# Kernel optimization log

Measured on AMD Instinct MI355X. Metric: run time of the kernel, lower is better.

Reference implementation:

```python
import jax, jax.numpy as jnp
import numpy as np

B, T, X, H, Z = 64, 2048, 128, 256, 64


def setup_inputs() -> dict:
    key = jax.random.key(0)
    ks = jax.random.split(key, 6)
    s = lambda n: 1.0 / np.sqrt(n).astype(np.float32)
    return {
        "x_seq": jax.random.normal(ks[0], (B, T, X), jnp.float32),
        # LSTMCell params packed as [i|f|g|o] gates. Flax: input dense has no bias,
        # hidden dense has bias.
        "Wi": jax.random.normal(ks[1], (X, 4 * H), jnp.float32) * s(X),
        "Wh": jax.random.normal(ks[2], (H, 4 * H), jnp.float32) * s(H),
        "bh": jnp.zeros((4 * H,), jnp.float32),
        # head: Dense(H) -> relu -> Dense(2Z)
        "W1": jax.random.normal(ks[3], (H, H), jnp.float32) * s(H),
        "b1": jnp.zeros((H,), jnp.float32),
        "W2": jax.random.normal(ks[4], (H, 2 * Z), jnp.float32) * s(H),
        "b2": jnp.zeros((2 * Z,), jnp.float32),
    }


def _forward(x_seq, Wi, Wh, bh, W1, b1, W2, b2):
    Bsz = x_seq.shape[0]
    Hd = Wh.shape[0]
    # Precompute input projection for all timesteps (one big GEMM).
    x_proj = jnp.einsum('btx,xg->btg', x_seq, Wi)  # (B, T, 4H)
    xp = jnp.swapaxes(x_proj, 0, 1)  # (T, B, 4H) for scan

    def step(carry, xp_t):
        c, h = carry
        gates = xp_t + h @ Wh + bh  # (B, 4H)
        i, f, g, o = jnp.split(gates, 4, axis=-1)
        i = jax.nn.sigmoid(i)
        f = jax.nn.sigmoid(f)
        g = jnp.tanh(g)
        o = jax.nn.sigmoid(o)
        c = f * c + i * g
        h = o * jnp.tanh(c)
        hid = jax.nn.relu(h @ W1 + b1)
        out = hid @ W2 + b2  # (B, 2Z)
        return (c, h), out

    c0 = jnp.zeros((Bsz, Hd), x_seq.dtype)
    h0 = jnp.zeros((Bsz, Hd), x_seq.dtype)
    _, outs = jax.lax.scan(step, (c0, h0), xp)  # outs: (T, B, 2Z)
    outs = jnp.swapaxes(outs, 0, 1)  # (B, T, 2Z)
    mu_seq, log_sigma_seq = jnp.split(outs, 2, axis=-1)
    return mu_seq, log_sigma_seq


def reference(x_seq, Wi, Wh, bh, W1, b1, W2, b2):
    return _forward(x_seq, Wi, Wh, bh, W1, b1, W2, b2)
```

## Files before the change

### kernel.cpp

```cpp
#include <hip/hip_runtime.h>

typedef _Float16 f16;
typedef _Float16 h2 __attribute__((ext_vector_type(2)));
typedef _Float16 h8 __attribute__((ext_vector_type(8)));
typedef float f4 __attribute__((ext_vector_type(4)));

constexpr int Bb = 64, Tt = 2048, Xx = 128, Hh = 256, G4 = 1024, Z2 = 128;

__device__ __forceinline__ float fdot2f(h2 a, h2 b, float c) {
#if __has_builtin(__builtin_amdgcn_fdot2)
  return __builtin_amdgcn_fdot2(a, b, c, false);
#else
  return c + (float)a[0] * (float)b[0] + (float)a[1] * (float)b[1];
#endif
}
__device__ __forceinline__ float tanhf_(float x) {
  float e = __expf(2.0f * x);
  return 1.0f - 2.0f * __builtin_amdgcn_rcpf(e + 1.0f);
}
__device__ __forceinline__ h2 bch2(unsigned int u) { return __builtin_bit_cast(h2, u); }

template <int CTRL>
__device__ __forceinline__ float qb(float v) {
  return __builtin_bit_cast(float,
      __builtin_amdgcn_mov_dpp(__builtin_bit_cast(int, v), CTRL, 0xf, 0xf, true));
}

__global__ void cast_f16_k(const float* __restrict__ in, f16* __restrict__ out, int n) {
  int i = (blockIdx.x * 256 + threadIdx.x) * 4;
  if (i >= n) return;
  float4 v = *(const float4*)(in + i);
  h2 a = {(f16)v.x, (f16)v.y};
  h2 b = {(f16)v.z, (f16)v.w};
  uint2 o = {__builtin_bit_cast(unsigned int, a), __builtin_bit_cast(unsigned int, b)};
  *(uint2*)(out + i) = o;
}

__global__ void cast_whT2_k(const float* __restrict__ Wh, f16* __restrict__ WhT2) {
  int idx = blockIdx.x * 256 + threadIdx.x;
  int tid = idx >> 9, f = idx & 511;
  int s = f >> 1, e = f & 1;
  int c_off, k;
  if (s < 96)      { c_off = 0; k = 2 * s + e; }
  else if (s < 192){ c_off = 1; k = 2 * (s - 96) + e; }
  else if (s < 224){ c_off = 0; k = 192 + 2 * (s - 192) + e; }
  else             { c_off = 1; k = 192 + 2 * (s - 224) + e; }
  int cc = 2 * tid + c_off;
  int j = cc >> 2, g = cc & 3;
  WhT2[(long)tid * 512 + f] = (f16)Wh[(long)k * G4 + g * 256 + j];
}

__global__ void cast_whT4_k(const float* __restrict__ Wh, f16* __restrict__ WhT4) {
  int idx = blockIdx.x * 256 + threadIdx.x;
  int tid = idx >> 9, f = idx & 511;
  int s = f >> 1, e = f & 1;
  int i = s >> 4, g = (s >> 2) & 3, m = s & 3;
  int j = tid >> 1, hf = tid & 1;
  int k = 128 * hf + 8 * i + 2 * m + e;
  WhT4[(long)tid * 512 + f] = (f16)Wh[(long)k * G4 + g * 256 + j];
}

__global__ __launch_bounds__(256, 4) void gemm_f16_k(
    const f16* __restrict__ A, const f16* __restrict__ Bm, const float* __restrict__ bias,
    f16* __restrict__ C16, float* __restrict__ Cmu, float* __restrict__ Cls,
    int N, int K, int a_shift, int a_ostride, int a_t0,
    int mode, int o_t0, int tcshift)
{
  __shared__ __align__(16) f16 At[64][48];
  __shared__ __align__(16) f16 Bt[64][48];
  const int tid = threadIdx.x;
  const int mblk = blockIdx.x, nblk = blockIdx.y;
  const int w = tid >> 6, lane = tid & 63;

  const int sa_row = tid >> 2, sa_k = (tid & 3) * 8;
  const int m_g = mblk * 64 + sa_row;
  const long arow = (long)(m_g >> a_shift) * a_ostride + a_t0 + (m_g & ((1 << a_shift) - 1));
  const f16* aptr = A + arow * K + sa_k;
  const int sb_k = tid >> 3, sb_n = (tid & 7) * 8;
  const f16* bptr = Bm + (long)sb_k * N + nblk * 64 + sb_n;

  f4 acc[4];
#pragma unroll
  for (int i = 0; i < 4; ++i) acc[i] = (f4){0.f, 0.f, 0.f, 0.f};

  const int arow_l = w * 16 + (lane & 15);
  const int k0 = (lane >> 4) * 8;

  for (int kk = 0; kk < K; kk += 32) {
    uint4 av = *(const uint4*)(aptr + kk);
    uint4 bv = *(const uint4*)(bptr + (long)kk * N);
    __syncthreads();
    *(uint4*)&At[sa_row][sa_k] = av;
    h8 bx = __builtin_bit_cast(h8, bv);
#pragma unroll
    for (int j = 0; j < 8; ++j) Bt[sb_n + j][sb_k] = bx[j];
    __syncthreads();
    h8 af = *(const h8*)&At[arow_l][k0];
#pragma unroll
    for (int nt = 0; nt < 4; ++nt) {
      h8 bf = *(const h8*)&Bt[nt * 16 + (lane & 15)][k0];
      acc[nt] = __builtin_amdgcn_mfma_f32_16x16x32_f16(af, bf, acc[nt], 0, 0, 0);
    }
  }

  const int row_l = w * 16 + ((lane >> 4) << 2);
  const int col_l = lane & 15;
#pragma unroll
  for (int nt = 0; nt < 4; ++nt) {
    int gcol = nblk * 64 + nt * 16 + col_l;
    float bv = bias[gcol];
#pragma unroll
    for (int r = 0; r < 4; ++r) {
      int gm = mblk * 64 + row_l + r;
      float val = acc[nt][r] + bv;
      if (mode == 1) val = fmaxf(val, 0.f);
      if (mode <= 1) {
        C16[(long)gm * N + gcol] = (f16)val;
      } else {
        int bb = gm >> tcshift, tl = gm & ((1 << tcshift) - 1);
        long orow = (long)bb * Tt + o_t0 + tl;
        if (gcol < 64) Cmu[orow * 64 + gcol] = val;
        else Cls[orow * 64 + (gcol - 64)] = val;
      }
    }
  }
}

__global__ void __launch_bounds__(512, 2) lstm512h_k(
    const f16* __restrict__ WhT4, const f16* __restrict__ xp,
    f16* __restrict__ hout, float* __restrict__ c_state, f16* __restrict__ h_state,
    int TC, int first)
{
  const int b = blockIdx.x, tid = threadIdx.x;
  const int j = tid >> 1, hf = tid & 1;
  __shared__ __align__(16) h2 hbuf[2][128];
  __shared__ uint4 wt[16][512];

  h2 w[192];
  {
    const uint4* p4 = (const uint4*)(WhT4 + (long)tid * 512);
#pragma unroll
    for (int u = 0; u < 48; ++u) {
      uint4 v = p4[u];
      w[4 * u + 0] = bch2(v.x); w[4 * u + 1] = bch2(v.y);
      w[4 * u + 2] = bch2(v.z); w[4 * u + 3] = bch2(v.w);
    }
#pragma unroll
    for (int gg = 0; gg < 16; ++gg) wt[gg][tid] = p4[48 + gg];
  }

  float c = first ? 0.f : c_state[b * Hh + j];
  if (tid < 128) {
    h2 hz = {(f16)0.f, (f16)0.f};
    hbuf[0][tid] = first ? hz : ((const h2*)h_state)[b * 128 + tid];
  }
  __syncthreads();

  const f16* xptr = xp + (long)b * TC * G4 + j;
  const f16* xend = xptr + (long)(TC - 1) * G4;
  f16 xc0 = xptr[0], xc1 = xptr[256], xc2 = xptr[512], xc3 = xptr[768];
  int p = 0;
  for (int t = 0; t < TC; ++t) {
    const f16* xnp = (xptr == xend) ? xptr : xptr + G4;
    f16 xn0 = xnp[0], xn1 = xnp[256], xn2 = xnp[512], xn3 = xnp[768];

    float d0 = 0.f, d1 = 0.f, d2 = 0.f, d3 = 0.f;
    const uint4* hq = (const uint4*)&hbuf[p][0] + hf * 16;
#pragma unroll
    for (int i = 0; i < 12; ++i) {
      uint4 hv = hq[i];
      h2 h0 = bch2(hv.x), h1 = bch2(hv.y), h2_ = bch2(hv.z), h3 = bch2(hv.w);
      d0 = fdot2f(w[16 * i + 0], h0, d0);  d0 = fdot2f(w[16 * i + 1], h1, d0);
      d0 = fdot2f(w[16 * i + 2], h2_, d0); d0 = fdot2f(w[16 * i + 3], h3, d0);
      d1 = fdot2f(w[16 * i + 4], h0, d1);  d1 = fdot2f(w[16 * i + 5], h1, d1);
      d1 = fdot2f(w[16 * i + 6], h2_, d1); d1 = fdot2f(w[16 * i + 7], h3, d1);
      d2 = fdot2f(w[16 * i + 8], h0, d2);  d2 = fdot2f(w[16 * i + 9], h1, d2);
      d2 = fdot2f(w[16 * i + 10], h2_, d2); d2 = fdot2f(w[16 * i + 11], h3, d2);
      d3 = fdot2f(w[16 * i + 12], h0, d3);  d3 = fdot2f(w[16 * i + 13], h1, d3);
      d3 = fdot2f(w[16 * i + 14], h2_, d3); d3 = fdot2f(w[16 * i + 15], h3, d3);
    }
#pragma unroll
    for (int i = 12; i < 16; ++i) {
      uint4 hv = hq[i];
      h2 h0 = bch2(hv.x), h1 = bch2(hv.y), h2_ = bch2(hv.z), h3 = bch2(hv.w);
      uint4 w0 = wt[(i - 12) * 4 + 0][tid];
      uint4 w1 = wt[(i - 12) * 4 + 1][tid];
      uint4 w2 = wt[(i - 12) * 4 + 2][tid];
      uint4 w3 = wt[(i - 12) * 4 + 3][tid];
      d0 = fdot2f(bch2(w0.x), h0, d0); d0 = fdot2f(bch2(w0.y), h1, d0);
      d0 = fdot2f(bch2(w0.z), h2_, d0); d0 = fdot2f(bch2(w0.w), h3, d0);
      d1 = fdot2f(bch2(w1.x), h0, d1); d1 = fdot2f(bch2(w1.y), h1, d1);
      d1 = fdot2f(bch2(w1.z), h2_, d1); d1 = fdot2f(bch2(w1.w), h3, d1);
      d2 = fdot2f(bch2(w2.x), h0, d2); d2 = fdot2f(bch2(w2.y), h1, d2);
      d2 = fdot2f(bch2(w2.z), h2_, d2); d2 = fdot2f(bch2(w2.w), h3, d2);
      d3 = fdot2f(bch2(w3.x), h0, d3); d3 = fdot2f(bch2(w3.y), h1, d3);
      d3 = fdot2f(bch2(w3.z), h2_, d3); d3 = fdot2f(bch2(w3.w), h3, d3);
    }

    d0 += qb<0xB1>(d0); d1 += qb<0xB1>(d1);
    d2 += qb<0xB1>(d2); d3 += qb<0xB1>(d3);

    float ti = d0 + (float)xc0, tf = d1 + (float)xc1;
    float tg = d2 + (float)xc2, to = d3 + (float)xc3;
    float ai = __builtin_amdgcn_rcpf(1.0f + __expf(-ti));
    float af = __builtin_amdgcn_rcpf(1.0f + __expf(-tf));
    float ag = 1.0f - 2.0f * __builtin_amdgcn_rcpf(1.0f + __expf(2.0f * tg));
    float ao = __builtin_amdgcn_rcpf(1.0f + __expf(-to));
    c = af * c + ai * ag;
    float hval = ao * tanhf_(c);
    if (!hf) {
      f16 hh = (f16)hval;
      ((f16*)&hbuf[p ^ 1][0])[j] = hh;
      hout[((long)b * TC + t) * Hh + j] = hh;
    }
    __syncthreads();
    p ^= 1;
    xc0 = xn0; xc1 = xn1; xc2 = xn2; xc3 = xn3;
    xptr = xnp;
  }
  if (!hf) c_state[b * Hh + j] = c;
  if (tid < 128) ((h2*)h_state)[b * 128 + tid] = hbuf[p][tid];
}

__global__ void __launch_bounds__(512, 2) lstm512_k(
    const f16* __restrict__ WhT2, const f16* __restrict__ xp,
    f16* __restrict__ hout, float* __restrict__ c_state, f16* __restrict__ h_state,
    int TC, int first)
{
  const int b = blockIdx.x, tid = threadIdx.x;
  const int j = tid >> 1, odd = tid & 1;
  __shared__ __align__(16) h2 hbuf[2][128];
  __shared__ uint4 wt[16][512];

  h2 w[192];
  {
    const uint4* p4 = (const uint4*)(WhT2 + (long)tid * 512);
#pragma unroll
    for (int u = 0; u < 48; ++u) {
      uint4 v = p4[u];
      w[4 * u + 0] = bch2(v.x); w[4 * u + 1] = bch2(v.y);
      w[4 * u + 2] = bch2(v.z); w[4 * u + 3] = bch2(v.w);
    }
#pragma unroll
    for (int gg = 0; gg < 16; ++gg) wt[gg][tid] = p4[48 + gg];
  }

  float c = first ? 0.f : c_state[b * Hh + j];
  if (tid < 128) {
    h2 hz = {(f16)0.f, (f16)0.f};
    hbuf[0][tid] = first ? hz : ((const h2*)h_state)[b * 128 + tid];
  }
  __syncthreads();

  const float sgn0 = odd ? 2.0f : -1.0f;
  const int xcol0 = (odd * 2) * 256 + j;
  const int xcol1 = xcol0 + 256;
  const f16* xbase = xp + (long)b * TC * G4;
  const f16* xptr0 = xbase + xcol0;
  const f16* xptr1 = xbase + xcol1;
  const f16* xend0 = xptr0 + (long)(TC - 1) * G4;
  f16 xc0 = *xptr0, xc1 = *xptr1;
  int p = 0;
  for (int t = 0; t < TC; ++t) {
    bool last = (xptr0 == xend0);
    const f16* xn0p = last ? xptr0 : xptr0 + G4;
    const f16* xn1p = last ? xptr1 : xptr1 + G4;
    f16 xn0 = *xn0p, xn1 = *xn1p;

    float a0 = (float)xc0, b0 = 0.f, a1 = (float)xc1, b1 = 0.f;
    const uint4* hb4 = (const uint4*)&hbuf[p][0];
#pragma unroll
    for (int i = 0; i < 24; ++i) {
      uint4 hv = hb4[i];
      a0 = fdot2f(w[4 * i + 0], bch2(hv.x), a0);
      b0 = fdot2f(w[4 * i + 1], bch2(hv.y), b0);
      a0 = fdot2f(w[4 * i + 2], bch2(hv.z), a0);
      b0 = fdot2f(w[4 * i + 3], bch2(hv.w), b0);
      a1 = fdot2f(w[96 + 4 * i + 0], bch2(hv.x), a1);
      b1 = fdot2f(w[96 + 4 * i + 1], bch2(hv.y), b1);
      a1 = fdot2f(w[96 + 4 * i + 2], bch2(hv.z), a1);
      b1 = fdot2f(w[96 + 4 * i + 3], bch2(hv.w), b1);
    }
#pragma unroll
    for (int gg = 0; gg < 8; ++gg) {
      uint4 hv = hb4[24 + gg];
      uint4 wa = wt[gg][tid];
      uint4 wb = wt[8 + gg][tid];
      a0 = fdot2f(bch2(wa.x), bch2(hv.x), a0);
      b0 = fdot2f(bch2(wa.y), bch2(hv.y), b0);
      a0 = fdot2f(bch2(wa.z), bch2(hv.z), a0);
      b0 = fdot2f(bch2(wa.w), bch2(hv.w), b0);
      a1 = fdot2f(bch2(wb.x), bch2(hv.x), a1);
      b1 = fdot2f(bch2(wb.y), bch2(hv.y), b1);
      a1 = fdot2f(bch2(wb.z), bch2(hv.z), a1);
      b1 = fdot2f(bch2(wb.w), bch2(hv.w), b1);
    }
    float A0 = a0 + b0, A1 = a1 + b1;

    float e0 = __expf(sgn0 * A0);
    float r0 = __builtin_amdgcn_rcpf(1.0f + e0);
    float act0 = odd ? 1.0f - 2.0f * r0 : r0;
    float e1 = __expf(-A1);
    float act1 = __builtin_amdgcn_rcpf(1.0f + e1);

    float px0 = qb<0xB1>(act0), px1 = qb<0xB1>(act1);
    float ai = odd ? px0 : act0;
    float af = odd ? px1 : act1;
    float ag = odd ? act0 : px0;
    float ao = odd ? act1 : px1;
    c = af * c + ai * ag;
    float hval = ao * tanhf_(c);
    if (!odd) {
      f16 hh = (f16)hval;
      ((f16*)&hbuf[p ^ 1][0])[j] = hh;
      hout[((long)b * TC + t) * Hh + j] = hh;
    }
    __syncthreads();
    p ^= 1;
    xc0 = xn0; xc1 = xn1;
    xptr0 = xn0p; xptr1 = xn1p;
  }
  if (!odd) c_state[b * Hh + j] = c;
  if (tid < 128) ((h2*)h_state)[b * 128 + tid] = hbuf[p][tid];
}

extern "C" void kernel_launch(void* const* d_in, const int* in_sizes, int n_in,
                              void* d_out, int out_size, void* d_ws, size_t ws_size,
                              hipStream_t stream)
{
  const float* x  = (const float*)d_in[0];
  const float* Wi = (const float*)d_in[1];
  const float* Wh = (const float*)d_in[2];
  const float* bh = (const float*)d_in[3];
  const float* W1 = (const float*)d_in[4];
  const float* b1 = (const float*)d_in[5];
  const float* W2 = (const float*)d_in[6];
  const float* b2 = (const float*)d_in[7];
  float* out = (float*)d_out;

  char* ws = (char*)d_ws;
  size_t off = 0;
  auto alloc = [&](size_t bytes) -> char* {
    char* p = ws + off;
    off = (off + bytes + 255) & ~(size_t)255;
    return p;
  };
  f16* x16   = (f16*)alloc((size_t)Bb * Tt * Xx * 2);
  f16* wi16  = (f16*)alloc((size_t)Xx * G4 * 2);
  f16* whT2  = (f16*)alloc((size_t)G4 * Hh * 2);
  f16* whT4  = (f16*)alloc((size_t)G4 * Hh * 2);
  f16* w116  = (f16*)alloc((size_t)Hh * Hh * 2);
  f16* w216  = (f16*)alloc((size_t)Hh * Z2 * 2);
  float* cst = (float*)alloc((size_t)Bb * Hh * 4);
  f16* hst   = (f16*)alloc((size_t)Bb * Hh * 2);

  int tc = 1024;
  while (tc > 32) {
    size_t need = (size_t)Bb * tc * G4 * 2 + (size_t)Bb * tc * Hh * 2;
    if (off + need <= ws_size) break;
    tc >>= 1;
  }
  int tcsh = __builtin_ctz((unsigned)tc);
  f16* xp16 = (f16*)alloc((size_t)Bb * tc * G4 * 2);
  f16* h16  = (f16*)alloc((size_t)Bb * tc * Hh * 2);
  f16* hid16 = xp16;

  cast_f16_k<<<(Bb * Tt * Xx) / 1024, 256, 0, stream>>>(x, x16, Bb * Tt * Xx);
  cast_f16_k<<<(Xx * G4) / 1024, 256, 0, stream>>>(Wi, wi16, Xx * G4);
  cast_f16_k<<<(Hh * Hh) / 1024, 256, 0, stream>>>(W1, w116, Hh * Hh);
  cast_f16_k<<<(Hh * Z2) / 1024, 256, 0, stream>>>(W2, w216, Hh * Z2);
  cast_whT2_k<<<(Hh * G4) / 256, 256, 0, stream>>>(Wh, whT2);
  cast_whT4_k<<<(Hh * G4) / 256, 256, 0, stream>>>(Wh, whT4);

  float* mu = out;
  float* ls = out + (size_t)Bb * Tt * 64;

  int ci = 0;
  for (int t0 = 0; t0 < Tt; t0 += tc, ++ci) {
    dim3 gx(Bb * tc / 64, G4 / 64);
    gemm_f16_k<<<gx, 256, 0, stream>>>(x16, wi16, bh, xp16, nullptr, nullptr,
                                       G4, Xx, tcsh, Tt, t0, 0, 0, 0);
    if (ci == 0)
      lstm512h_k<<<Bb, 512, 0, stream>>>(whT4, xp16, h16, cst, hst, tc, (t0 == 0) ? 1 : 0);
    else
      lstm512_k<<<Bb, 512, 0, stream>>>(whT2, xp16, h16, cst, hst, tc, (t0 == 0) ? 1 : 0);
    dim3 g1g(Bb * tc / 64, Hh / 64);
    gemm_f16_k<<<g1g, 256, 0, stream>>>(h16, w116, b1, hid16, nullptr, nullptr,
                                        Hh, Hh, 30, 0, 0, 1, 0, 0);
    dim3 g2g(Bb * tc / 64, Z2 / 64);
    gemm_f16_k<<<g2g, 256, 0, stream>>>(hid16, w216, b2, nullptr, mu, ls,
                                        Z2, Hh, 30, 0, 0, 2, t0, tcsh);
  }
}
```

Baseline: 3.224 ms.

## Stream LSTM weight tail from global, interleave gate columns, pad h buffer

The input projection weights and bias are permuted so the four gate pre-activations for each hidden unit sit next to each other, letting the recurrent kernel load them with one 8-byte read. A new first-chunk LSTM kernel keeps 160 weight pairs in registers and streams the remaining weights from global memory with software prefetch instead of shared memory, which lowers register and LDS pressure. The hidden-state LDS buffer is padded to avoid bank conflicts between the two half-threads, and the old odd/even gate-split kernel is replaced by the padded 4-gate kernel for later chunks. The risk is that the per-step global weight loads add latency on the serial critical path.

```diff
diff --git a/kernel.cpp b/kernel.cpp
--- a/kernel.cpp
+++ b/kernel.cpp
@@ -36,18 +36,14 @@
   *(uint2*)(out + i) = o;
 }
 
-__global__ void cast_whT2_k(const float* __restrict__ Wh, f16* __restrict__ WhT2) {
+__global__ void cast_wiP_k(const float* __restrict__ Wi, f16* __restrict__ out) {
   int idx = blockIdx.x * 256 + threadIdx.x;
-  int tid = idx >> 9, f = idx & 511;
-  int s = f >> 1, e = f & 1;
-  int c_off, k;
-  if (s < 96)      { c_off = 0; k = 2 * s + e; }
-  else if (s < 192){ c_off = 1; k = 2 * (s - 96) + e; }
-  else if (s < 224){ c_off = 0; k = 192 + 2 * (s - 192) + e; }
-  else             { c_off = 1; k = 192 + 2 * (s - 224) + e; }
-  int cc = 2 * tid + c_off;
-  int j = cc >> 2, g = cc & 3;
-  WhT2[(long)tid * 512 + f] = (f16)Wh[(long)k * G4 + g * 256 + j];
+  int k = idx >> 10, cp = idx & 1023;
+  out[idx] = (f16)Wi[(long)k * G4 + (cp & 3) * 256 + (cp >> 2)];
+}
+__global__ void cast_bhp_k(const float* __restrict__ bh, float* __restrict__ bhp) {
+  int cp = blockIdx.x * 256 + threadIdx.x;
+  bhp[cp] = bh[(cp & 3) * 256 + (cp >> 2)];
 }
 
 __global__ void cast_whT4_k(const float* __restrict__ Wh, f16* __restrict__ WhT4) {
@@ -58,6 +54,28 @@
   int j = tid >> 1, hf = tid & 1;
   int k = 128 * hf + 8 * i + 2 * m + e;
   WhT4[(long)tid * 512 + f] = (f16)Wh[(long)k * G4 + g * 256 + j];
+}
+
+__global__ void cast_whT5_k(const float* __restrict__ Wh,
+                            f16* __restrict__ Wh5h, f16* __restrict__ wtail) {
+  int idx = blockIdx.x * 256 + threadIdx.x;
+  if (idx < 512 * 320) {
+    int tid = idx / 320, f = idx % 320;
+    int s = f >> 1, e = f & 1;
+    int i = s >> 4, g = (s >> 2) & 3, m = s & 3;
+    int j = tid >> 1, hf = tid & 1;
+    int k = 128 * hf + 8 * i + 2 * m + e;
+    Wh5h[idx] = (f16)Wh[(long)k * G4 + g * 256 + j];
+  } else {
+    int r = idx - 512 * 320;
+    int u4 = r >> 3, me = r & 7;
+    int m = me >> 1, e = me & 1;
+    int ip = u4 >> 9, tid = u4 & 511;
+    int i = 10 + (ip >> 2), g = ip & 3;
+    int j = tid >> 1, hf = tid & 1;
+    int k = 128 * hf + 8 * i + 2 * m + e;
+    wtail[r] = (f16)Wh[(long)k * G4 + g * 256 + j];
+  }
 }
 
 __global__ __launch_bounds__(256, 4) void gemm_f16_k(
@@ -126,14 +144,118 @@
   }
 }
 
-__global__ void __launch_bounds__(512, 2) lstm512h_k(
+
+__global__ void __launch_bounds__(512, 2) lstm512s_k(
+    const f16* __restrict__ Wh5h, const f16* __restrict__ wtail,
+    const f16* __restrict__ xp, f16* __restrict__ hout,
+    float* __restrict__ c_state, f16* __restrict__ h_state, int TC, int first)
+{
+  const int b = blockIdx.x, tid = threadIdx.x;
+  const int j = tid >> 1, hf = tid & 1;
+  __shared__ __align__(16) h2 hbuf[2][136];
+
+  h2 w[160];
+  {
+    const uint4* p4 = (const uint4*)(Wh5h + (long)tid * 320);
+#pragma unroll
+    for (int u = 0; u < 40; ++u) {
+      uint4 v = p4[u];
+      w[4 * u + 0] = bch2(v.x); w[4 * u + 1] = bch2(v.y);
+      w[4 * u + 2] = bch2(v.z); w[4 * u + 3] = bch2(v.w);
+    }
+  }
+  const uint4* tp = (const uint4*)wtail + tid;
+
+  float c = first ? 0.f : c_state[b * Hh + j];
+  if (tid < 128) {
+    h2 hz = {(f16)0.f, (f16)0.f};
+    hbuf[0][tid + ((tid >> 6) << 2)] =
+        first ? hz : ((const h2*)h_state)[b * 128 + tid];
+  }
+  __syncthreads();
+
+  const f16* xptr = xp + (long)b * TC * G4 + 4 * j;
+  const f16* xend = xptr + (long)(TC - 1) * G4;
+  uint2 xv = *(const uint2*)xptr;
+  int p = 0;
+  for (int t = 0; t < TC; ++t) {
+    const f16* xnp = (xptr == xend) ? xptr : xptr + G4;
+    uint2 xn = *(const uint2*)xnp;
+
+    uint4 A0 = tp[0], A1 = tp[512], A2 = tp[1024], A3 = tp[1536];
+    uint4 B0 = tp[2048], B1 = tp[2560], B2 = tp[3072], B3 = tp[3584];
+
+    const uint4* hq = (const uint4*)&hbuf[p][0] + hf * 17;
+    float d0 = 0.f, d1 = 0.f, d2 = 0.f, d3 = 0.f;
+#pragma unroll
+    for (int i = 0; i < 10; ++i) {
+      uint4 hv = hq[i];
+      h2 h0 = bch2(hv.x), h1 = bch2(hv.y), h2_ = bch2(hv.z), h3 = bch2(hv.w);
+      d0 = fdot2f(w[16 * i + 0], h0, d0);   d0 = fdot2f(w[16 * i + 1], h1, d0);
+      d0 = fdot2f(w[16 * i + 2], h2_, d0);  d0 = fdot2f(w[16 * i + 3], h3, d0);
+      d1 = fdot2f(w[16 * i + 4], h0, d1);   d1 = fdot2f(w[16 * i + 5], h1, d1);
+      d1 = fdot2f(w[16 * i + 6], h2_, d1);  d1 = fdot2f(w[16 * i + 7], h3, d1);
+      d2 = fdot2f(w[16 * i + 8], h0, d2);   d2 = fdot2f(w[16 * i + 9], h1, d2);
+      d2 = fdot2f(w[16 * i + 10], h2_, d2); d2 = fdot2f(w[16 * i + 11], h3, d2);
+      d3 = fdot2f(w[16 * i + 12], h0, d3);  d3 = fdot2f(w[16 * i + 13], h1, d3);
+      d3 = fdot2f(w[16 * i + 14], h2_, d3); d3 = fdot2f(w[16 * i + 15], h3, d3);
+    }
+#pragma unroll
+    for (int ii = 0; ii < 6; ++ii) {
+      uint4 C0 = {0, 0, 0, 0}, C1 = C0, C2 = C0, C3 = C0;
+      if (ii < 4) {
+        const uint4* np = tp + (size_t)(4 * (ii + 2)) * 512;
+        C0 = np[0]; C1 = np[512]; C2 = np[1024]; C3 = np[1536];
+      }
+      uint4 hv = hq[10 + ii];
+      h2 h0 = bch2(hv.x), h1 = bch2(hv.y), h2_ = bch2(hv.z), h3 = bch2(hv.w);
+      d0 = fdot2f(bch2(A0.x), h0, d0); d0 = fdot2f(bch2(A0.y), h1, d0);
+      d0 = fdot2f(bch2(A0.z), h2_, d0); d0 = fdot2f(bch2(A0.w), h3, d0);
+      d1 = fdot2f(bch2(A1.x), h0, d1); d1 = fdot2f(bch2(A1.y), h1, d1);
+      d1 = fdot2f(bch2(A1.z), h2_, d1); d1 = fdot2f(bch2(A1.w), h3, d1);
+      d2 = fdot2f(bch2(A2.x), h0, d2); d2 = fdot2f(bch2(A2.y), h1, d2);
+      d2 = fdot2f(bch2(A2.z), h2_, d2); d2 = fdot2f(bch2(A2.w), h3, d2);
+      d3 = fdot2f(bch2(A3.x), h0, d3); d3 = fdot2f(bch2(A3.y), h1, d3);
+      d3 = fdot2f(bch2(A3.z), h2_, d3); d3 = fdot2f(bch2(A3.w), h3, d3);
+      A0 = B0; A1 = B1; A2 = B2; A3 = B3;
+      B0 = C0; B1 = C1; B2 = C2; B3 = C3;
+    }
+
+    d0 += qb<0xB1>(d0); d1 += qb<0xB1>(d1);
+    d2 += qb<0xB1>(d2); d3 += qb<0xB1>(d3);
+
+    h2 xlo = bch2(xv.x), xhi = bch2(xv.y);
+    float ti = d0 + (float)xlo[0], tf = d1 + (float)xlo[1];
+    float tg = d2 + (float)xhi[0], to = d3 + (float)xhi[1];
+    float ai = __builtin_amdgcn_rcpf(1.0f + __expf(-ti));
+    float af = __builtin_amdgcn_rcpf(1.0f + __expf(-tf));
+    float ag = 1.0f - 2.0f * __builtin_amdgcn_rcpf(1.0f + __expf(2.0f * tg));
+    float ao = __builtin_amdgcn_rcpf(1.0f + __expf(-to));
+    c = af * c + ai * ag;
+    float hval = ao * tanhf_(c);
+    if (!hf) {
+      f16 hh = (f16)hval;
+      ((f16*)&hbuf[p ^ 1][0])[j + ((j >> 7) << 3)] = hh;
+      hout[((long)b * TC + t) * Hh + j] = hh;
+    }
+    __syncthreads();
+    p ^= 1;
+    xv = xn;
+    xptr = xnp;
+  }
+  if (!hf) c_state[b * Hh + j] = c;
+  if (tid < 128)
+    ((h2*)h_state)[b * 128 + tid] = hbuf[p][tid + ((tid >> 6) << 2)];
+}
+
+__global__ void __launch_bounds__(512, 2) lstm512hf_k(
     const f16* __restrict__ WhT4, const f16* __restrict__ xp,
     f16* __restrict__ hout, float* __restrict__ c_state, f16* __restrict__ h_state,
     int TC, int first)
 {
   const int b = blockIdx.x, tid = threadIdx.x;
   const int j = tid >> 1, hf = tid & 1;
-  __shared__ __align__(16) h2 hbuf[2][128];
+  __shared__ __align__(16) h2 hbuf[2][136];
   __shared__ uint4 wt[16][512];
 
   h2 w[192];
@@ -152,29 +274,30 @@
   float c = first ? 0.f : c_state[b * Hh + j];
   if (tid < 128) {
     h2 hz = {(f16)0.f, (f16)0.f};
-    hbuf[0][tid] = first ? hz : ((const h2*)h_state)[b * 128 + tid];
+    hbuf[0][tid + ((tid >> 6) << 2)] =
+        first ? hz : ((const h2*)h_state)[b * 128 + tid];
   }
   __syncthreads();
 
-  const f16* xptr = xp + (long)b * TC * G4 + j;
+  const f16* xptr = xp + (long)b * TC * G4 + 4 * j;
   const f16* xend = xptr + (long)(TC - 1) * G4;
-  f16 xc0 = xptr[0], xc1 = xptr[256], xc2 = xptr[512], xc3 = xptr[768];
+  uint2 xv = *(const uint2*)xptr;
   int p = 0;
   for (int t = 0; t < TC; ++t) {
     const f16* xnp = (xptr == xend) ? xptr : xptr + G4;
-    f16 xn0 = xnp[0], xn1 = xnp[256], xn2 = xnp[512], xn3 = xnp[768];
+    uint2 xn = *(const uint2*)xnp;
 
     float d0 = 0.f, d1 = 0.f, d2 = 0.f, d3 = 0.f;
-    const uint4* hq = (const uint4*)&hbuf[p][0] + hf * 16;
+    const uint4* hq = (const uint4*)&hbuf[p][0] + hf * 17;
 #pragma unroll
     for (int i = 0; i < 12; ++i) {
       uint4 hv = hq[i];
       h2 h0 = bch2(hv.x), h1 = bch2(hv.y), h2_ = bch2(hv.z), h3 = bch2(hv.w);
-      d0 = fdot2f(w[16 * i + 0], h0, d0);  d0 = fdot2f(w[16 * i + 1], h1, d0);
-      d0 = fdot2f(w[16 * i + 2], h2_, d0); d0 = fdot2f(w[16 * i + 3], h3, d0);
-      d1 = fdot2f(w[16 * i + 4], h0, d1);  d1 = fdot2f(w[16 * i + 5], h1, d1);
-      d1 = fdot2f(w[16 * i + 6], h2_, d1); d1 = fdot2f(w[16 * i + 7], h3, d1);
-      d2 = fdot2f(w[16 * i + 8], h0, d2);  d2 = fdot2f(w[16 * i + 9], h1, d2);
+      d0 = fdot2f(w[16 * i + 0], h0, d0);   d0 = fdot2f(w[16 * i + 1], h1, d0);
+      d0 = fdot2f(w[16 * i + 2], h2_, d0);  d0 = fdot2f(w[16 * i + 3], h3, d0);
+      d1 = fdot2f(w[16 * i + 4], h0, d1);   d1 = fdot2f(w[16 * i + 5], h1, d1);
+      d1 = fdot2f(w[16 * i + 6], h2_, d1);  d1 = fdot2f(w[16 * i + 7], h3, d1);
+      d2 = fdot2f(w[16 * i + 8], h0, d2);   d2 = fdot2f(w[16 * i + 9], h1, d2);
       d2 = fdot2f(w[16 * i + 10], h2_, d2); d2 = fdot2f(w[16 * i + 11], h3, d2);
       d3 = fdot2f(w[16 * i + 12], h0, d3);  d3 = fdot2f(w[16 * i + 13], h1, d3);
       d3 = fdot2f(w[16 * i + 14], h2_, d3); d3 = fdot2f(w[16 * i + 15], h3, d3);
@@ -200,8 +323,9 @@
     d0 += qb<0xB1>(d0); d1 += qb<0xB1>(d1);
     d2 += qb<0xB1>(d2); d3 += qb<0xB1>(d3);
 
-    float ti = d0 + (float)xc0, tf = d1 + (float)xc1;
-    float tg = d2 + (float)xc2, to = d3 + (float)xc3;
+    h2 xlo = bch2(xv.x), xhi = bch2(xv.y);
+    float ti = d0 + (float)xlo[0], tf = d1 + (float)xlo[1];
+    float tg = d2 + (float)xhi[0], to = d3 + (float)xhi[1];
     float ai = __builtin_amdgcn_rcpf(1.0f + __expf(-ti));
     float af = __builtin_amdgcn_rcpf(1.0f + __expf(-tf));
     float ag = 1.0f - 2.0f * __builtin_amdgcn_rcpf(1.0f + __expf(2.0f * tg));
@@ -210,118 +334,17 @@
     float hval = ao * tanhf_(c);
     if (!hf) {
       f16 hh = (f16)hval;
-      ((f16*)&hbuf[p ^ 1][0])[j] = hh;
+      ((f16*)&hbuf[p ^ 1][0])[j + ((j >> 7) << 3)] = hh;
       hout[((long)b * TC + t) * Hh + j] = hh;
     }
     __syncthreads();
     p ^= 1;
-    xc0 = xn0; xc1 = xn1; xc2 = xn2; xc3 = xn3;
+    xv = xn;
     xptr = xnp;
   }
   if (!hf) c_state[b * Hh + j] = c;
-  if (tid < 128) ((h2*)h_state)[b * 128 + tid] = hbuf[p][tid];
-}
-
-__global__ void __launch_bounds__(512, 2) lstm512_k(
-    const f16* __restrict__ WhT2, const f16* __restrict__ xp,
-    f16* __restrict__ hout, float* __restrict__ c_state, f16* __restrict__ h_state,
-    int TC, int first)
-{
-  const int b = blockIdx.x, tid = threadIdx.x;
-  const int j = tid >> 1, odd = tid & 1;
-  __shared__ __align__(16) h2 hbuf[2][128];
-  __shared__ uint4 wt[16][512];
-
-  h2 w[192];
-  {
-    const uint4* p4 = (const uint4*)(WhT2 + (long)tid * 512);
-#pragma unroll
-    for (int u = 0; u < 48; ++u) {
-      uint4 v = p4[u];
-      w[4 * u + 0] = bch2(v.x); w[4 * u + 1] = bch2(v.y);
-      w[4 * u + 2] = bch2(v.z); w[4 * u + 3] = bch2(v.w);
-    }
-#pragma unroll
-    for (int gg = 0; gg < 16; ++gg) wt[gg][tid] = p4[48 + gg];
-  }
-
-  float c = first ? 0.f : c_state[b * Hh + j];
-  if (tid < 128) {
-    h2 hz = {(f16)0.f, (f16)0.f};
-    hbuf[0][tid] = first ? hz : ((const h2*)h_state)[b * 128 + tid];
-  }
-  __syncthreads();
-
-  const float sgn0 = odd ? 2.0f : -1.0f;
-  const int xcol0 = (odd * 2) * 256 + j;
-  const int xcol1 = xcol0 + 256;
-  const f16* xbase = xp + (long)b * TC * G4;
-  const f16* xptr0 = xbase + xcol0;
-  const f16* xptr1 = xbase + xcol1;
-  const f16* xend0 = xptr0 + (long)(TC - 1) * G4;
-  f16 xc0 = *xptr0, xc1 = *xptr1;
-  int p = 0;
-  for (int t = 0; t < TC; ++t) {
-    bool last = (xptr0 == xend0);
-    const f16* xn0p = last ? xptr0 : xptr0 + G4;
-    const f16* xn1p = last ? xptr1 : xptr1 + G4;
-    f16 xn0 = *xn0p, xn1 = *xn1p;
-
-    float a0 = (float)xc0, b0 = 0.f, a1 = (float)xc1, b1 = 0.f;
-    const uint4* hb4 = (const uint4*)&hbuf[p][0];
-#pragma unroll
-    for (int i = 0; i < 24; ++i) {
-      uint4 hv = hb4[i];
-      a0 = fdot2f(w[4 * i + 0], bch2(hv.x), a0);
-      b0 = fdot2f(w[4 * i + 1], bch2(hv.y), b0);
-      a0 = fdot2f(w[4 * i + 2], bch2(hv.z), a0);
-      b0 = fdot2f(w[4 * i + 3], bch2(hv.w), b0);
-      a1 = fdot2f(w[96 + 4 * i + 0], bch2(hv.x), a1);
-      b1 = fdot2f(w[96 + 4 * i + 1], bch2(hv.y), b1);
-      a1 = fdot2f(w[96 + 4 * i + 2], bch2(hv.z), a1);
-      b1 = fdot2f(w[96 + 4 * i + 3], bch2(hv.w), b1);
-    }
-#pragma unroll
-    for (int gg = 0; gg < 8; ++gg) {
-      uint4 hv = hb4[24 + gg];
-      uint4 wa = wt[gg][tid];
-      uint4 wb = wt[8 + gg][tid];
-      a0 = fdot2f(bch2(wa.x), bch2(hv.x), a0);
-      b0 = fdot2f(bch2(wa.y), bch2(hv.y), b0);
-      a0 = fdot2f(bch2(wa.z), bch2(hv.z), a0);
-      b0 = fdot2f(bch2(wa.w), bch2(hv.w), b0);
-      a1 = fdot2f(bch2(wb.x), bch2(hv.x), a1);
-      b1 = fdot2f(bch2(wb.y), bch2(hv.y), b1);
-      a1 = fdot2f(bch2(wb.z), bch2(hv.z), a1);
-      b1 = fdot2f(bch2(wb.w), bch2(hv.w), b1);
-    }
-    float A0 = a0 + b0, A1 = a1 + b1;
-
-    float e0 = __expf(sgn0 * A0);
-    float r0 = __builtin_amdgcn_rcpf(1.0f + e0);
-    float act0 = odd ? 1.0f - 2.0f * r0 : r0;
-    float e1 = __expf(-A1);
-    float act1 = __builtin_amdgcn_rcpf(1.0f + e1);
-
-    float px0 = qb<0xB1>(act0), px1 = qb<0xB1>(act1);
-    float ai = odd ? px0 : act0;
-    float af = odd ? px1 : act1;
-    float ag = odd ? act0 : px0;
-    float ao = odd ? act1 : px1;
-    c = af * c + ai * ag;
-    float hval = ao * tanhf_(c);
-    if (!odd) {
-      f16 hh = (f16)hval;
-      ((f16*)&hbuf[p ^ 1][0])[j] = hh;
-      hout[((long)b * TC + t) * Hh + j] = hh;
-    }
-    __syncthreads();
-    p ^= 1;
-    xc0 = xn0; xc1 = xn1;
-    xptr0 = xn0p; xptr1 = xn1p;
-  }
-  if (!odd) c_state[b * Hh + j] = c;
-  if (tid < 128) ((h2*)h_state)[b * 128 + tid] = hbuf[p][tid];
+  if (tid < 128)
+    ((h2*)h_state)[b * 128 + tid] = hbuf[p][tid + ((tid >> 6) << 2)];
 }
 
 extern "C" void kernel_launch(void* const* d_in, const int* in_sizes, int n_in,
@@ -345,14 +368,16 @@
     off = (off + bytes + 255) & ~(size_t)255;
     return p;
   };
-  f16* x16   = (f16*)alloc((size_t)Bb * Tt * Xx * 2);
-  f16* wi16  = (f16*)alloc((size_t)Xx * G4 * 2);
-  f16* whT2  = (f16*)alloc((size_t)G4 * Hh * 2);
-  f16* whT4  = (f16*)alloc((size_t)G4 * Hh * 2);
-  f16* w116  = (f16*)alloc((size_t)Hh * Hh * 2);
-  f16* w216  = (f16*)alloc((size_t)Hh * Z2 * 2);
-  float* cst = (float*)alloc((size_t)Bb * Hh * 4);
-  f16* hst   = (f16*)alloc((size_t)Bb * Hh * 2);
+  f16* x16    = (f16*)alloc((size_t)Bb * Tt * Xx * 2);
+  f16* wi16p  = (f16*)alloc((size_t)Xx * G4 * 2);
+  float* bhp  = (float*)alloc((size_t)G4 * 4);
+  f16* whT4   = (f16*)alloc((size_t)G4 * Hh * 2);
+  f16* wh5h   = (f16*)alloc((size_t)512 * 320 * 2);
+  f16* wtail  = (f16*)alloc((size_t)24 * 512 * 8 * 2);
+  f16* w116   = (f16*)alloc((size_t)Hh * Hh * 2);
+  f16* w216   = (f16*)alloc((size_t)Hh * Z2 * 2);
+  float* cst  = (float*)alloc((size_t)Bb * Hh * 4);
+  f16* hst    = (f16*)alloc((size_t)Bb * Hh * 2);
 
   int tc = 1024;
   while (tc > 32) {
@@ -366,11 +391,12 @@
   f16* hid16 = xp16;
 
   cast_f16_k<<<(Bb * Tt * Xx) / 1024, 256, 0, stream>>>(x, x16, Bb * Tt * Xx);
-  cast_f16_k<<<(Xx * G4) / 1024, 256, 0, stream>>>(Wi, wi16, Xx * G4);
+  cast_wiP_k<<<(Xx * G4) / 256, 256, 0, stream>>>(Wi, wi16p);
+  cast_bhp_k<<<4, 256, 0, stream>>>(bh, bhp);
   cast_f16_k<<<(Hh * Hh) / 1024, 256, 0, stream>>>(W1, w116, Hh * Hh);
   cast_f16_k<<<(Hh * Z2) / 1024, 256, 0, stream>>>(W2, w216, Hh * Z2);
-  cast_whT2_k<<<(Hh * G4) / 256, 256, 0, stream>>>(Wh, whT2);
   cast_whT4_k<<<(Hh * G4) / 256, 256, 0, stream>>>(Wh, whT4);
+  cast_whT5_k<<<(Hh * G4) / 256, 256, 0, stream>>>(Wh, wh5h, wtail);
 
   float* mu = out;
   float* ls = out + (size_t)Bb * Tt * 64;
@@ -378,12 +404,14 @@
   int ci = 0;
   for (int t0 = 0; t0 < Tt; t0 += tc, ++ci) {
     dim3 gx(Bb * tc / 64, G4 / 64);
-    gemm_f16_k<<<gx, 256, 0, stream>>>(x16, wi16, bh, xp16, nullptr, nullptr,
+    gemm_f16_k<<<gx, 256, 0, stream>>>(x16, wi16p, bhp, xp16, nullptr, nullptr,
                                        G4, Xx, tcsh, Tt, t0, 0, 0, 0);
     if (ci == 0)
-      lstm512h_k<<<Bb, 512, 0, stream>>>(whT4, xp16, h16, cst, hst, tc, (t0 == 0) ? 1 : 0);
+      lstm512s_k<<<Bb, 512, 0, stream>>>(wh5h, wtail, xp16, h16, cst, hst, tc,
+                                         (t0 == 0) ? 1 : 0);
     else
-      lstm512_k<<<Bb, 512, 0, stream>>>(whT2, xp16, h16, cst, hst, tc, (t0 == 0) ? 1 : 0);
+      lstm512hf_k<<<Bb, 512, 0, stream>>>(whT4, xp16, h16, cst, hst, tc,
+                                          (t0 == 0) ? 1 : 0);
     dim3 g1g(Bb * tc / 64, Hh / 64);
     gemm_f16_k<<<g1g, 256, 0, stream>>>(h16, w116, b1, hid16, nullptr, nullptr,
                                         Hh, Hh, 30, 0, 0, 1, 0, 0);
```

Measured after the change: 5.340 ms. +65.6%, slower.

## Interleave gate columns and use one-thread-per-hidden-unit LSTM kernel for first chunk

Applied to the files above, without the earlier changes.

Permutes Wi and bh so the input-projection GEMM writes the four gates of each hidden unit contiguously, letting LSTM kernels load gate inputs with a single vector load instead of strided scalar loads. Replaces the first-chunk 512-thread split-K kernel (which needed a DPP cross-lane reduction) with a 256-thread kernel where each thread owns a full hidden unit: 384 register h2 weights plus 32 rows in LDS. This removes the partial-sum reduction and halves thread count, but doubles per-thread register pressure and serial dot-product length per step, which may cause spills or longer step latency.

```diff
diff --git a/kernel.cpp b/kernel.cpp
--- a/kernel.cpp
+++ b/kernel.cpp
@@ -34,6 +34,16 @@
   h2 b = {(f16)v.z, (f16)v.w};
   uint2 o = {__builtin_bit_cast(unsigned int, a), __builtin_bit_cast(unsigned int, b)};
   *(uint2*)(out + i) = o;
+}
+
+__global__ void cast_wiP_k(const float* __restrict__ Wi, f16* __restrict__ out) {
+  int idx = blockIdx.x * 256 + threadIdx.x;
+  int k = idx >> 10, cp = idx & 1023;
+  out[idx] = (f16)Wi[(long)k * G4 + (cp & 3) * 256 + (cp >> 2)];
+}
+__global__ void cast_bhp_k(const float* __restrict__ bh, float* __restrict__ bhp) {
+  int cp = blockIdx.x * 256 + threadIdx.x;
+  bhp[cp] = bh[(cp & 3) * 256 + (cp >> 2)];
 }
 
 __global__ void cast_whT2_k(const float* __restrict__ Wh, f16* __restrict__ WhT2) {
@@ -50,14 +60,13 @@
   WhT2[(long)tid * 512 + f] = (f16)Wh[(long)k * G4 + g * 256 + j];
 }
 
-__global__ void cast_whT4_k(const float* __restrict__ Wh, f16* __restrict__ WhT4) {
+__global__ void cast_whT6_k(const float* __restrict__ Wh, f16* __restrict__ WhT6) {
   int idx = blockIdx.x * 256 + threadIdx.x;
-  int tid = idx >> 9, f = idx & 511;
+  int tid = idx >> 10, f = idx & 1023;
   int s = f >> 1, e = f & 1;
   int i = s >> 4, g = (s >> 2) & 3, m = s & 3;
-  int j = tid >> 1, hf = tid & 1;
-  int k = 128 * hf + 8 * i + 2 * m + e;
-  WhT4[(long)tid * 512 + f] = (f16)Wh[(long)k * G4 + g * 256 + j];
+  int k = 8 * i + 2 * m + e;
+  WhT6[idx] = (f16)Wh[(long)k * G4 + g * 256 + tid];
 }
 
 __global__ __launch_bounds__(256, 4) void gemm_f16_k(
@@ -126,67 +135,66 @@
   }
 }
 
-__global__ void __launch_bounds__(512, 2) lstm512h_k(
-    const f16* __restrict__ WhT4, const f16* __restrict__ xp,
+__global__ void __launch_bounds__(256, 1) lstm256_k(
+    const f16* __restrict__ WhT6, const f16* __restrict__ xp,
     f16* __restrict__ hout, float* __restrict__ c_state, f16* __restrict__ h_state,
     int TC, int first)
 {
   const int b = blockIdx.x, tid = threadIdx.x;
-  const int j = tid >> 1, hf = tid & 1;
   __shared__ __align__(16) h2 hbuf[2][128];
-  __shared__ uint4 wt[16][512];
-
-  h2 w[192];
+  __shared__ uint4 wt[32][256];
+
+  h2 w[384];
   {
-    const uint4* p4 = (const uint4*)(WhT4 + (long)tid * 512);
-#pragma unroll
-    for (int u = 0; u < 48; ++u) {
+    const uint4* p4 = (const uint4*)(WhT6 + (long)tid * 1024);
+#pragma unroll
+    for (int u = 0; u < 96; ++u) {
       uint4 v = p4[u];
       w[4 * u + 0] = bch2(v.x); w[4 * u + 1] = bch2(v.y);
       w[4 * u + 2] = bch2(v.z); w[4 * u + 3] = bch2(v.w);
     }
 #pragma unroll
-    for (int gg = 0; gg < 16; ++gg) wt[gg][tid] = p4[48 + gg];
-  }
-
-  float c = first ? 0.f : c_state[b * Hh + j];
+    for (int r = 0; r < 32; ++r) wt[r][tid] = p4[96 + r];
+  }
+
+  float c = first ? 0.f : c_state[b * Hh + tid];
   if (tid < 128) {
     h2 hz = {(f16)0.f, (f16)0.f};
     hbuf[0][tid] = first ? hz : ((const h2*)h_state)[b * 128 + tid];
   }
   __syncthreads();
 
-  const f16* xptr = xp + (long)b * TC * G4 + j;
+  const f16* xptr = xp + (long)b * TC * G4 + 4 * tid;
   const f16* xend = xptr + (long)(TC - 1) * G4;
-  f16 xc0 = xptr[0], xc1 = xptr[256], xc2 = xptr[512], xc3 = xptr[768];
+  uint2 xv = *(const uint2*)xptr;
   int p = 0;
   for (int t = 0; t < TC; ++t) {
     const f16* xnp = (xptr == xend) ? xptr : xptr + G4;
-    f16 xn0 = xnp[0], xn1 = xnp[256], xn2 = xnp[512], xn3 = xnp[768];
+    uint2 xn = *(const uint2*)xnp;
 
     float d0 = 0.f, d1 = 0.f, d2 = 0.f, d3 = 0.f;
-    const uint4* hq = (const uint4*)&hbuf[p][0] + hf * 16;
-#pragma unroll
-    for (int i = 0; i < 12; ++i) {
-      uint4 hv = hq[i];
+    const uint4* hb4 = (const uint4*)&hbuf[p][0];
+#pragma unroll
+    for (int ii = 0; ii < 24; ++ii) {
+      uint4 hv = hb4[ii];
       h2 h0 = bch2(hv.x), h1 = bch2(hv.y), h2_ = bch2(hv.z), h3 = bch2(hv.w);
-      d0 = fdot2f(w[16 * i + 0], h0, d0);  d0 = fdot2f(w[16 * i + 1], h1, d0);
-      d0 = fdot2f(w[16 * i + 2], h2_, d0); d0 = fdot2f(w[16 * i + 3], h3, d0);
-      d1 = fdot2f(w[16 * i + 4], h0, d1);  d1 = fdot2f(w[16 * i + 5], h1, d1);
-      d1 = fdot2f(w[16 * i + 6], h2_, d1); d1 = fdot2f(w[16 * i + 7], h3, d1);
-      d2 = fdot2f(w[16 * i + 8], h0, d2);  d2 = fdot2f(w[16 * i + 9], h1, d2);
-      d2 = fdot2f(w[16 * i + 10], h2_, d2); d2 = fdot2f(w[16 * i + 11], h3, d2);
-      d3 = fdot2f(w[16 * i + 12], h0, d3);  d3 = fdot2f(w[16 * i + 13], h1, d3);
-      d3 = fdot2f(w[16 * i + 14], h2_, d3); d3 = fdot2f(w[16 * i + 15], h3, d3);
-    }
-#pragma unroll
-    for (int i = 12; i < 16; ++i) {
-      uint4 hv = hq[i];
+      d0 = fdot2f(w[16 * ii + 0], h0, d0);  d0 = fdot2f(w[16 * ii + 1], h1, d0);
+      d0 = fdot2f(w[16 * ii + 2], h2_, d0); d0 = fdot2f(w[16 * ii + 3], h3, d0);
+      d1 = fdot2f(w[16 * ii + 4], h0, d1);  d1 = fdot2f(w[16 * ii + 5], h1, d1);
+      d1 = fdot2f(w[16 * ii + 6], h2_, d1); d1 = fdot2f(w[16 * ii + 7], h3, d1);
+      d2 = fdot2f(w[16 * ii + 8], h0, d2);  d2 = fdot2f(w[16 * ii + 9], h1, d2);
+      d2 = fdot2f(w[16 * ii + 10], h2_, d2); d2 = fdot2f(w[16 * ii + 11], h3, d2);
+      d3 = fdot2f(w[16 * ii + 12], h0, d3);  d3 = fdot2f(w[16 * ii + 13], h1, d3);
+      d3 = fdot2f(w[16 * ii + 14], h2_, d3); d3 = fdot2f(w[16 * ii + 15], h3, d3);
+    }
+#pragma unroll
+    for (int ii = 24; ii < 32; ++ii) {
+      uint4 hv = hb4[ii];
       h2 h0 = bch2(hv.x), h1 = bch2(hv.y), h2_ = bch2(hv.z), h3 = bch2(hv.w);
-      uint4 w0 = wt[(i - 12) * 4 + 0][tid];
-      uint4 w1 = wt[(i - 12) * 4 + 1][tid];
-      uint4 w2 = wt[(i - 12) * 4 + 2][tid];
-      uint4 w3 = wt[(i - 12) * 4 + 3][tid];
+      uint4 w0 = wt[(ii - 24) * 4 + 0][tid];
+      uint4 w1 = wt[(ii - 24) * 4 + 1][tid];
+      uint4 w2 = wt[(ii - 24) * 4 + 2][tid];
+      uint4 w3 = wt[(ii - 24) * 4 + 3][tid];
       d0 = fdot2f(bch2(w0.x), h0, d0); d0 = fdot2f(bch2(w0.y), h1, d0);
       d0 = fdot2f(bch2(w0.z), h2_, d0); d0 = fdot2f(bch2(w0.w), h3, d0);
       d1 = fdot2f(bch2(w1.x), h0, d1); d1 = fdot2f(bch2(w1.y), h1, d1);
@@ -197,28 +205,24 @@
       d3 = fdot2f(bch2(w3.z), h2_, d3); d3 = fdot2f(bch2(w3.w), h3, d3);
     }
 
-    d0 += qb<0xB1>(d0); d1 += qb<0xB1>(d1);
-    d2 += qb<0xB1>(d2); d3 += qb<0xB1>(d3);
-
-    float ti = d0 + (float)xc0, tf = d1 + (float)xc1;
-    float tg = d2 + (float)xc2, to = d3 + (float)xc3;
+    h2 xlo = bch2(xv.x), xhi = bch2(xv.y);
+    float ti = d0 + (float)xlo[0], tf = d1 + (float)xlo[1];
+    float tg = d2 + (float)xhi[0], to = d3 + (float)xhi[1];
     float ai = __builtin_amdgcn_rcpf(1.0f + __expf(-ti));
     float af = __builtin_amdgcn_rcpf(1.0f + __expf(-tf));
     float ag = 1.0f - 2.0f * __builtin_amdgcn_rcpf(1.0f + __expf(2.0f * tg));
     float ao = __builtin_amdgcn_rcpf(1.0f + __expf(-to));
     c = af * c + ai * ag;
     float hval = ao * tanhf_(c);
-    if (!hf) {
-      f16 hh = (f16)hval;
-      ((f16*)&hbuf[p ^ 1][0])[j] = hh;
-      hout[((long)b * TC + t) * Hh + j] = hh;
-    }
+    f16 hh = (f16)hval;
+    ((f16*)&hbuf[p ^ 1][0])[tid] = hh;
+    hout[((long)b * TC + t) * Hh + tid] = hh;
     __syncthreads();
     p ^= 1;
-    xc0 = xn0; xc1 = xn1; xc2 = xn2; xc3 = xn3;
+    xv = xn;
     xptr = xnp;
   }
-  if (!hf) c_state[b * Hh + j] = c;
+  c_state[b * Hh + tid] = c;
   if (tid < 128) ((h2*)h_state)[b * 128 + tid] = hbuf[p][tid];
 }
 
@@ -253,21 +257,15 @@
   __syncthreads();
 
   const float sgn0 = odd ? 2.0f : -1.0f;
-  const int xcol0 = (odd * 2) * 256 + j;
-  const int xcol1 = xcol0 + 256;
-  const f16* xbase = xp + (long)b * TC * G4;
-  const f16* xptr0 = xbase + xcol0;
-  const f16* xptr1 = xbase + xcol1;
-  const f16* xend0 = xptr0 + (long)(TC - 1) * G4;
-  f16 xc0 = *xptr0, xc1 = *xptr1;
+  const f16* xptr = xp + (long)b * TC * G4 + 2 * tid;
+  const f16* xend = xptr + (long)(TC - 1) * G4;
+  h2 xv = *(const h2*)xptr;
   int p = 0;
   for (int t = 0; t < TC; ++t) {
-    bool last = (xptr0 == xend0);
-    const f16* xn0p = last ? xptr0 : xptr0 + G4;
-    const f16* xn1p = last ? xptr1 : xptr1 + G4;
-    f16 xn0 = *xn0p, xn1 = *xn1p;
-
-    float a0 = (float)xc0, b0 = 0.f, a1 = (float)xc1, b1 = 0.f;
+    const f16* xnp = (xptr == xend) ? xptr : xptr + G4;
+    h2 xn = *(const h2*)xnp;
+
+    float a0 = (float)xv[0], b0 = 0.f, a1 = (float)xv[1], b1 = 0.f;
     const uint4* hb4 = (const uint4*)&hbuf[p][0];
 #pragma unroll
     for (int i = 0; i < 24; ++i) {
@@ -317,8 +315,8 @@
     }
     __syncthreads();
     p ^= 1;
-    xc0 = xn0; xc1 = xn1;
-    xptr0 = xn0p; xptr1 = xn1p;
+    xv = xn;
+    xptr = xnp;
   }
   if (!odd) c_state[b * Hh + j] = c;
   if (tid < 128) ((h2*)h_state)[b * 128 + tid] = hbuf[p][tid];
@@ -345,14 +343,15 @@
     off = (off + bytes + 255) & ~(size_t)255;
     return p;
   };
-  f16* x16   = (f16*)alloc((size_t)Bb * Tt * Xx * 2);
-  f16* wi16  = (f16*)alloc((size_t)Xx * G4 * 2);
-  f16* whT2  = (f16*)alloc((size_t)G4 * Hh * 2);
-  f16* whT4  = (f16*)alloc((size_t)G4 * Hh * 2);
-  f16* w116  = (f16*)alloc((size_t)Hh * Hh * 2);
-  f16* w216  = (f16*)alloc((size_t)Hh * Z2 * 2);
-  float* cst = (float*)alloc((size_t)Bb * Hh * 4);
-  f16* hst   = (f16*)alloc((size_t)Bb * Hh * 2);
+  f16* x16    = (f16*)alloc((size_t)Bb * Tt * Xx * 2);
+  f16* wi16p  = (f16*)alloc((size_t)Xx * G4 * 2);
+  float* bhp  = (float*)alloc((size_t)G4 * 4);
+  f16* whT2   = (f16*)alloc((size_t)G4 * Hh * 2);
+  f16* whT6   = (f16*)alloc((size_t)G4 * Hh * 2);
+  f16* w116   = (f16*)alloc((size_t)Hh * Hh * 2);
+  f16* w216   = (f16*)alloc((size_t)Hh * Z2 * 2);
+  float* cst  = (float*)alloc((size_t)Bb * Hh * 4);
+  f16* hst    = (f16*)alloc((size_t)Bb * Hh * 2);
 
   int tc = 1024;
   while (tc > 32) {
@@ -366,11 +365,12 @@
   f16* hid16 = xp16;
 
   cast_f16_k<<<(Bb * Tt * Xx) / 1024, 256, 0, stream>>>(x, x16, Bb * Tt * Xx);
-  cast_f16_k<<<(Xx * G4) / 1024, 256, 0, stream>>>(Wi, wi16, Xx * G4);
+  cast_wiP_k<<<(Xx * G4) / 256, 256, 0, stream>>>(Wi, wi16p);
+  cast_bhp_k<<<4, 256, 0, stream>>>(bh, bhp);
   cast_f16_k<<<(Hh * Hh) / 1024, 256, 0, stream>>>(W1, w116, Hh * Hh);
   cast_f16_k<<<(Hh * Z2) / 1024, 256, 0, stream>>>(W2, w216, Hh * Z2);
   cast_whT2_k<<<(Hh * G4) / 256, 256, 0, stream>>>(Wh, whT2);
-  cast_whT4_k<<<(Hh * G4) / 256, 256, 0, stream>>>(Wh, whT4);
+  cast_whT6_k<<<(Hh * G4) / 256, 256, 0, stream>>>(Wh, whT6);
 
   float* mu = out;
   float* ls = out + (size_t)Bb * Tt * 64;
@@ -378,10 +378,10 @@
   int ci = 0;
   for (int t0 = 0; t0 < Tt; t0 += tc, ++ci) {
     dim3 gx(Bb * tc / 64, G4 / 64);
-    gemm_f16_k<<<gx, 256, 0, stream>>>(x16, wi16, bh, xp16, nullptr, nullptr,
+    gemm_f16_k<<<gx, 256, 0, stream>>>(x16, wi16p, bhp, xp16, nullptr, nullptr,
                                        G4, Xx, tcsh, Tt, t0, 0, 0, 0);
     if (ci == 0)
-      lstm512h_k<<<Bb, 512, 0, stream>>>(whT4, xp16, h16, cst, hst, tc, (t0 == 0) ? 1 : 0);
+      lstm256_k<<<Bb, 256, 0, stream>>>(whT6, xp16, h16, cst, hst, tc, (t0 == 0) ? 1 : 0);
     else
       lstm512_k<<<Bb, 512, 0, stream>>>(whT2, xp16, h16, cst, hst, tc, (t0 == 0) ? 1 : 0);
     dim3 g1g(Bb * tc / 64, Hh / 64);
```

Measured after the change: 4.628 ms. +43.5%, slower.
